# Kernel tuning notes

Measured on AMD Instinct MI355X. Metric: run time of the kernel, lower is better.

The kernel has to match this reference:

```python
import jax, jax.numpy as jnp
import numpy as np

N_HEADS = 16

def setup_inputs() -> dict:
    key = jax.random.key(0)
    ks = jax.random.split(key, 9)
    B, T, C = 2, 2048, 1024
    s = 1.0 / np.sqrt(C)
    return {
        "x": jax.random.normal(ks[0], (B, T, C), dtype=jnp.float32),
        "Wq": jax.random.normal(ks[1], (C, C), dtype=jnp.float32) * s,
        "bq": jax.random.normal(ks[2], (C,), dtype=jnp.float32) * s,
        "Wk": jax.random.normal(ks[3], (C, C), dtype=jnp.float32) * s,
        "bk": jax.random.normal(ks[4], (C,), dtype=jnp.float32) * s,
        "Wv": jax.random.normal(ks[5], (C, C), dtype=jnp.float32) * s,
        "bv": jax.random.normal(ks[6], (C,), dtype=jnp.float32) * s,
        "Wo": jax.random.normal(ks[7], (C, C), dtype=jnp.float32) * s,
        "bo": jax.random.normal(ks[8], (C,), dtype=jnp.float32) * s,
    }

def reference(x, Wq, bq, Wk, bk, Wv, bv, Wo, bo):
    B, T, C = x.shape
    H = N_HEADS
    d = C // H
    # projections -> [B, H, T, d]
    def proj(W, b):
        return (x @ W + b).reshape(B, T, H, d).transpose(0, 2, 1, 3)
    Q, K, V = proj(Wq, bq), proj(Wk, bk), proj(Wv, bv)
    scores = jnp.einsum('bhqd,bhkd->bhqk', Q, K) / jnp.sqrt(jnp.float32(d))
    causal = jnp.tril(jnp.ones((T, T), dtype=bool))  # keep lower triangle
    scores = jnp.where(causal, scores, jnp.finfo(scores.dtype).min)
    attn = jax.nn.softmax(scores, axis=-1)
    out = jnp.einsum('bhqk,bhkd->bhqd', attn, V)  # [B,H,T,d]
    out = out.transpose(0, 2, 1, 3).reshape(B, T, C)
    return out @ Wo + bo
```

## Files before the change

kernel.cpp:

```cpp
#include <hip/hip_runtime.h>
#include <stdint.h>

#define BB 2
#define TT 2048
#define CC 1024
#define HH 16
#define DD 64
#define MM (BB*TT)

typedef unsigned short u16;
typedef __attribute__((ext_vector_type(8))) short short8;
typedef __attribute__((ext_vector_type(4))) float float4v;
typedef __attribute__((ext_vector_type(16))) float f32x16;
typedef __attribute__((ext_vector_type(4))) unsigned short ushort4v;

typedef const __attribute__((address_space(1))) void* gas_t;
typedef __attribute__((address_space(3))) void* las_t;

__device__ __forceinline__ u16 f2bf(float f) {
  union { float f; uint32_t u; } v; v.f = f;
  uint32_t u = v.u;
  return (u16)((u + 0x7FFFu + ((u >> 16) & 1)) >> 16);
}

__device__ __forceinline__ uint32_t cvtpk(float lo, float hi) {
  uint32_t r;
  asm("v_cvt_pk_bf16_f32 %0, %1, %2" : "=v"(r) : "v"(lo), "v"(hi));
  return r;
}

__device__ __forceinline__ void gld_lds16(const void* g, void* l) {
  __builtin_amdgcn_global_load_lds((gas_t)g, (las_t)l, 16, 0, 0);
}

__global__ __launch_bounds__(256) void k_convert_x(const float* __restrict__ x, u16* __restrict__ xb) {
  int i = (blockIdx.x * 256 + threadIdx.x) * 4;
  float4v v = *(const float4v*)(x + i);
  ushort4v o;
  o[0] = f2bf(v[0]); o[1] = f2bf(v[1]); o[2] = f2bf(v[2]); o[3] = f2bf(v[3]);
  *(ushort4v*)(xb + i) = o;
}

__global__ __launch_bounds__(256) void k_transpose_w(const float* __restrict__ Wq, const float* __restrict__ Wk,
                                                     const float* __restrict__ Wv, const float* __restrict__ Wo,
                                                     u16* __restrict__ WT) {
  __shared__ u16 tile[64][72];
  int which = blockIdx.y;
  const float* W = (which == 0) ? Wq : (which == 1) ? Wk : (which == 2) ? Wv : Wo;
  u16* out = WT + (size_t)which * CC * CC;
  int tr = (blockIdx.x >> 4) * 64, tc = (blockIdx.x & 15) * 64;
#pragma unroll
  for (int i = 0; i < 16; ++i) {
    int e = i * 256 + threadIdx.x;
    int r = e >> 6, c = e & 63;
    tile[r][c] = f2bf(W[(size_t)(tr + r) * CC + tc + c]);
  }
  __syncthreads();
#pragma unroll
  for (int i = 0; i < 16; ++i) {
    int e = i * 256 + threadIdx.x;
    int cc2 = e >> 6, rr = e & 63;
    out[(size_t)(tc + cc2) * CC + tr + rr] = tile[rr][cc2];
  }
}

__global__ __launch_bounds__(256, 2) void k_qkv_gemm(
    const u16* __restrict__ xb, const u16* __restrict__ WTall,
    const float* __restrict__ bq, const float* __restrict__ bk, const float* __restrict__ bv,
    u16* __restrict__ Qw, u16* __restrict__ Kw, u16* __restrict__ Vtw) {
  __shared__ u16 Al[2][128 * 32];
  __shared__ u16 Bl[2][128 * 32];
  int p = blockIdx.y;
  const u16* WT = WTall + (size_t)p * (CC * CC);
  const float* bias = (p == 0) ? bq : (p == 1) ? bk : bv;
  int m0 = (blockIdx.x >> 3) * 128;
  int n0 = (blockIdx.x & 7) * 128;
  int tid = threadIdx.x;
  int lane = tid & 63, wave = tid >> 6;
  int wr = wave >> 1, wc = wave & 1;

  float4v acc[4][4];
#pragma unroll
  for (int i = 0; i < 4; ++i)
#pragma unroll
    for (int j = 0; j < 4; ++j) acc[i][j] = float4v{0.f, 0.f, 0.f, 0.f};

  auto stage = [&](int buf, int kt) {
    int k0 = kt * 32;
#pragma unroll
    for (int it = 0; it < 2; ++it) {
      int fc = tid + it * 256;
      int r = fc >> 2, c = fc & 3;
      int cg = c ^ ((r >> 1) & 3);
      const u16* gA = xb + (size_t)(m0 + r) * CC + k0 + cg * 8;
      const u16* gB = WT + (size_t)(n0 + r) * CC + k0 + cg * 8;
      char* lA = (char*)&Al[buf][0] + (wave * 64 + it * 256) * 16;
      char* lB = (char*)&Bl[buf][0] + (wave * 64 + it * 256) * 16;
      gld_lds16(gA, lA);
      gld_lds16(gB, lB);
    }
  };

  stage(0, 0);
  __syncthreads();
  int buf = 0;
  for (int kt = 0; kt < 32; ++kt) {
    if (kt + 1 < 32) stage(buf ^ 1, kt + 1);
    short8 af[4], bfr[4];
#pragma unroll
    for (int mf = 0; mf < 4; ++mf) {
      int row = wr * 64 + mf * 16 + (lane & 15);
      int cs = (lane >> 4) ^ ((row >> 1) & 3);
      af[mf] = *(const short8*)((const char*)&Al[buf][0] + row * 64 + cs * 16);
    }
#pragma unroll
    for (int nf = 0; nf < 4; ++nf) {
      int row = wc * 64 + nf * 16 + (lane & 15);
      int cs = (lane >> 4) ^ ((row >> 1) & 3);
      bfr[nf] = *(const short8*)((const char*)&Bl[buf][0] + row * 64 + cs * 16);
    }
#pragma unroll
    for (int mf = 0; mf < 4; ++mf)
#pragma unroll
      for (int nf = 0; nf < 4; ++nf)
        acc[mf][nf] = __builtin_amdgcn_mfma_f32_16x16x32_bf16(af[mf], bfr[nf], acc[mf][nf], 0, 0, 0);
    __syncthreads();
    buf ^= 1;
  }

  const float QSCALE = 0.125f * 1.44269504088896340736f;
#pragma unroll
  for (int mf = 0; mf < 4; ++mf) {
#pragma unroll
    for (int nf = 0; nf < 4; ++nf) {
      int n = n0 + wc * 64 + nf * 16 + (lane & 15);
      float bval = bias[n];
      int rowBase = wr * 64 + mf * 16 + (lane >> 4) * 4;
      int m_ = m0 + rowBase;
      int b_ = m_ >> 11, t_ = m_ & 2047;
      int h_ = n >> 6, dd = n & 63;
      if (p == 2) {
        ushort4v pk;
#pragma unroll
        for (int i = 0; i < 4; ++i) pk[i] = f2bf(acc[mf][nf][i] + bval);
        *(ushort4v*)(Vtw + ((size_t)(b_ * HH + h_) * DD + dd) * TT + t_) = pk;
      } else {
        u16* outp = (p == 0) ? Qw : Kw;
        float s = (p == 0) ? QSCALE : 1.0f;
#pragma unroll
        for (int i = 0; i < 4; ++i) {
          outp[((size_t)(b_ * HH + h_) * TT + (t_ + i)) * DD + dd] = f2bf((acc[mf][nf][i] + bval) * s);
        }
      }
    }
  }
}

__global__ __launch_bounds__(128, 2) void k_attn(
    const u16* __restrict__ Qw, const u16* __restrict__ Kw,
    const u16* __restrict__ Vtw, u16* __restrict__ Ow) {
  __shared__ u16 Klds[2][64 * 64];
  __shared__ u16 Vlds[2][64 * 64];
  int bid = blockIdx.x;
  int xcd = bid & 7, rank = bid >> 3;
  int bh = xcd + ((rank & 3) << 3);
  int u = 31 - (rank >> 2);
  int tid = threadIdx.x, lane = tid & 63, wave = tid >> 6;
  int l31 = lane & 31, hi = lane >> 5;
  int b_ = bh >> 4, h_ = bh & 15;
  const u16* Qbase = Qw + (size_t)bh * TT * DD;
  const u16* Kbase = Kw + (size_t)bh * TT * DD;
  const u16* Vbase = Vtw + (size_t)bh * DD * TT;
  int qw = u * 64 + wave * 32;
  int nt = u + 1;

  short8 qf[4];
#pragma unroll
  for (int ks = 0; ks < 4; ++ks)
    qf[ks] = *(const short8*)(Qbase + (size_t)(qw + l31) * DD + ks * 16 + hi * 8);

  int sr = tid >> 3;
  int sc = tid & 7;

  f32x16 acc0, acc1;
#pragma unroll
  for (int r = 0; r < 16; ++r) { acc0[r] = 0.f; acc1[r] = 0.f; }
  float mrun = -1e30f, lrun = 0.f;

  auto stageKV = [&](int t, int buf) {
    int kv0 = t * 64;
#pragma unroll
    for (int rd = 0; rd < 4; ++rd) {
      int r = rd * 16 + sr;
      int cg = sc ^ (r & 7);
      const u16* gK = Kbase + (size_t)(kv0 + r) * DD + cg * 8;
      const u16* gV = Vbase + (size_t)r * TT + kv0 + cg * 8;
      char* lK = (char*)&Klds[buf][0] + (rd * 128 + wave * 64) * 16;
      char* lV = (char*)&Vlds[buf][0] + (rd * 128 + wave * 64) * 16;
      gld_lds16(gK, lK);
      gld_lds16(gV, lV);
    }
  };

  stageKV(0, 0);
  int buf = 0;
  for (int t = 0; t < nt; ++t) {
    __syncthreads();
    if (t + 1 < nt) stageKV(t + 1, buf ^ 1);
    int kv0 = t * 64;
    const char* Kb = (const char*)&Klds[buf][0];
    const char* Vb = (const char*)&Vlds[buf][0];
    int swz = (l31 & 7);

    f32x16 s0, s1;
#pragma unroll
    for (int r = 0; r < 16; ++r) { s0[r] = 0.f; s1[r] = 0.f; }
#pragma unroll
    for (int ks = 0; ks < 4; ++ks) {
      short8 kf = *(const short8*)(Kb + l31 * 128 + ((2 * ks + hi) ^ swz) * 16);
      s0 = __builtin_amdgcn_mfma_f32_32x32x16_bf16(kf, qf[ks], s0, 0, 0, 0);
    }
#pragma unroll
    for (int ks = 0; ks < 4; ++ks) {
      short8 kf = *(const short8*)(Kb + (l31 + 32) * 128 + ((2 * ks + hi) ^ swz) * 16);
      s1 = __builtin_amdgcn_mfma_f32_32x32x16_bf16(kf, qf[ks], s1, 0, 0, 0);
    }

    if (kv0 + 63 > qw) {
      int qg = qw + l31;
#pragma unroll
      for (int r = 0; r < 16; ++r) {
        int kvg = kv0 + 8 * (r >> 2) + 4 * hi + (r & 3);
        if (kvg > qg) s0[r] = -1e30f;
        if (kvg + 32 > qg) s1[r] = -1e30f;
      }
    }

    float pm = -1e30f;
#pragma unroll
    for (int r = 0; r < 16; ++r) pm = fmaxf(pm, s0[r]);
#pragma unroll
    for (int r = 0; r < 16; ++r) pm = fmaxf(pm, s1[r]);
    pm = fmaxf(pm, __shfl_xor(pm, 32));

    if (__any(pm > mrun + 8.f)) {
      float mn = fmaxf(mrun, pm);
      float sc_ = __builtin_exp2f(mrun - mn);
      mrun = mn; lrun *= sc_;
#pragma unroll
      for (int r = 0; r < 16; ++r) { acc0[r] *= sc_; acc1[r] *= sc_; }
    }

    float rs = 0.f;
#pragma unroll
    for (int r = 0; r < 16; ++r) { s0[r] = __builtin_exp2f(s0[r] - mrun); rs += s0[r]; }
#pragma unroll
    for (int r = 0; r < 16; ++r) { s1[r] = __builtin_exp2f(s1[r] - mrun); rs += s1[r]; }
    rs += __shfl_xor(rs, 32);
    lrun += rs;

    uint32_t pk0[4][2], pk1[4][2];
#pragma unroll
    for (int m = 0; m < 4; ++m) {
      pk0[m][0] = cvtpk(s0[4 * m + 0], s0[4 * m + 1]);
      pk0[m][1] = cvtpk(s0[4 * m + 2], s0[4 * m + 3]);
      pk1[m][0] = cvtpk(s1[4 * m + 0], s1[4 * m + 1]);
      pk1[m][1] = cvtpk(s1[4 * m + 2], s1[4 * m + 3]);
    }

#define SLICE(PK, Q1, VS)                                                     \
    {                                                                         \
      uint32_t k0 = hi ? PK[2 * Q1 + 1][0] : PK[2 * Q1][0];                   \
      uint32_t k1 = hi ? PK[2 * Q1 + 1][1] : PK[2 * Q1][1];                   \
      uint32_t t0 = hi ? PK[2 * Q1][0] : PK[2 * Q1 + 1][0];                   \
      uint32_t t1 = hi ? PK[2 * Q1][1] : PK[2 * Q1 + 1][1];                   \
      uint32_t r0 = (uint32_t)__shfl_xor((int)t0, 32);                        \
      uint32_t r1 = (uint32_t)__shfl_xor((int)t1, 32);                        \
      union { uint32_t u[4]; short8 v; } pw;                                  \
      pw.u[0] = hi ? r0 : k0; pw.u[1] = hi ? r1 : k1;                         \
      pw.u[2] = hi ? k0 : r0; pw.u[3] = hi ? k1 : r1;                         \
      short8 vf0 = *(const short8*)(Vb + l31 * 128 + ((2 * VS + hi) ^ swz) * 16);       \
      short8 vf1 = *(const short8*)(Vb + (l31 + 32) * 128 + ((2 * VS + hi) ^ swz) * 16);\
      acc0 = __builtin_amdgcn_mfma_f32_32x32x16_bf16(vf0, pw.v, acc0, 0, 0, 0);         \
      acc1 = __builtin_amdgcn_mfma_f32_32x32x16_bf16(vf1, pw.v, acc1, 0, 0, 0);         \
    }
    SLICE(pk0, 0, 0)
    SLICE(pk0, 1, 1)
    SLICE(pk1, 0, 2)
    SLICE(pk1, 1, 3)
#undef SLICE
    buf ^= 1;
  }

  float inv = 1.f / lrun;
  int t_ = qw + l31;
  u16* orow = Ow + ((size_t)(b_ * TT + t_)) * CC + h_ * DD;
#pragma unroll
  for (int m = 0; m < 4; ++m) {
    ushort4v p0, p1;
#pragma unroll
    for (int j = 0; j < 4; ++j) {
      p0[j] = f2bf(acc0[4 * m + j] * inv);
      p1[j] = f2bf(acc1[4 * m + j] * inv);
    }
    *(ushort4v*)(orow + 8 * m + 4 * hi) = p0;
    *(ushort4v*)(orow + 32 + 8 * m + 4 * hi) = p1;
  }
}

__global__ __launch_bounds__(256, 2) void k_out_gemm(
    const u16* __restrict__ Ob, const u16* __restrict__ WoT,
    const float* __restrict__ bo, float* __restrict__ out) {
  __shared__ u16 Al[2][128 * 32];
  __shared__ u16 Bl[2][128 * 32];
  int m0 = (blockIdx.x >> 3) * 128;
  int n0 = (blockIdx.x & 7) * 128;
  int tid = threadIdx.x;
  int lane = tid & 63, wave = tid >> 6;
  int wr = wave >> 1, wc = wave & 1;

  float4v acc[4][4];
#pragma unroll
  for (int i = 0; i < 4; ++i)
#pragma unroll
    for (int j = 0; j < 4; ++j) acc[i][j] = float4v{0.f, 0.f, 0.f, 0.f};

  auto stage = [&](int buf, int kt) {
    int k0 = kt * 32;
#pragma unroll
    for (int it = 0; it < 2; ++it) {
      int fc = tid + it * 256;
      int r = fc >> 2, c = fc & 3;
      int cg = c ^ ((r >> 1) & 3);
      const u16* gA = Ob + (size_t)(m0 + r) * CC + k0 + cg * 8;
      const u16* gB = WoT + (size_t)(n0 + r) * CC + k0 + cg * 8;
      char* lA = (char*)&Al[buf][0] + (wave * 64 + it * 256) * 16;
      char* lB = (char*)&Bl[buf][0] + (wave * 64 + it * 256) * 16;
      gld_lds16(gA, lA);
      gld_lds16(gB, lB);
    }
  };

  stage(0, 0);
  __syncthreads();
  int buf = 0;
  for (int kt = 0; kt < 32; ++kt) {
    if (kt + 1 < 32) stage(buf ^ 1, kt + 1);
    short8 af[4], bfr[4];
#pragma unroll
    for (int mf = 0; mf < 4; ++mf) {
      int row = wr * 64 + mf * 16 + (lane & 15);
      int cs = (lane >> 4) ^ ((row >> 1) & 3);
      af[mf] = *(const short8*)((const char*)&Al[buf][0] + row * 64 + cs * 16);
    }
#pragma unroll
    for (int nf = 0; nf < 4; ++nf) {
      int row = wc * 64 + nf * 16 + (lane & 15);
      int cs = (lane >> 4) ^ ((row >> 1) & 3);
      bfr[nf] = *(const short8*)((const char*)&Bl[buf][0] + row * 64 + cs * 16);
    }
#pragma unroll
    for (int mf = 0; mf < 4; ++mf)
#pragma unroll
      for (int nf = 0; nf < 4; ++nf)
        acc[mf][nf] = __builtin_amdgcn_mfma_f32_16x16x32_bf16(af[mf], bfr[nf], acc[mf][nf], 0, 0, 0);
    __syncthreads();
    buf ^= 1;
  }

#pragma unroll
  for (int mf = 0; mf < 4; ++mf)
#pragma unroll
    for (int nf = 0; nf < 4; ++nf) {
      int n = n0 + wc * 64 + nf * 16 + (lane & 15);
      float bval = bo[n];
      int rowBase = m0 + wr * 64 + mf * 16 + (lane >> 4) * 4;
#pragma unroll
      for (int i = 0; i < 4; ++i)
        out[(size_t)(rowBase + i) * CC + n] = acc[mf][nf][i] + bval;
    }
}

extern "C" void kernel_launch(void* const* d_in, const int* in_sizes, int n_in,
                              void* d_out, int out_size, void* d_ws, size_t ws_size,
                              hipStream_t stream) {
  const float* x  = (const float*)d_in[0];
  const float* Wq = (const float*)d_in[1];
  const float* bq = (const float*)d_in[2];
  const float* Wk = (const float*)d_in[3];
  const float* bk = (const float*)d_in[4];
  const float* Wv = (const float*)d_in[5];
  const float* bv = (const float*)d_in[6];
  const float* Wo = (const float*)d_in[7];
  const float* bo = (const float*)d_in[8];
  float* out = (float*)d_out;
  char* ws = (char*)d_ws;
  if (ws_size < (size_t)50331648) return;

  u16* xb  = (u16*)(ws);
  u16* WT  = (u16*)(ws + 8388608);
  u16* Qw  = (u16*)(ws + 16777216);
  u16* Kw  = (u16*)(ws + 25165824);
  u16* Vtw = (u16*)(ws + 33554432);
  u16* Ob  = (u16*)(ws + 41943040);

  hipLaunchKernelGGL(k_convert_x, dim3(4096), dim3(256), 0, stream, x, xb);
  hipLaunchKernelGGL(k_transpose_w, dim3(256, 4), dim3(256), 0, stream, Wq, Wk, Wv, Wo, WT);
  hipLaunchKernelGGL(k_qkv_gemm, dim3(256, 3), dim3(256), 0, stream,
                     xb, WT, bq, bk, bv, Qw, Kw, Vtw);
  hipLaunchKernelGGL(k_attn, dim3(1024), dim3(128), 0, stream, Qw, Kw, Vtw, Ob);
  hipLaunchKernelGGL(k_out_gemm, dim3(256), dim3(256), 0, stream,
                     Ob, WT + 3 * 1048576, bo, out);
}
```

Before: 204.6 us.

## Split attention KV range across two wave pairs and merge partial softmax states

After: 215.0 us. 1.05x slower.

```diff
diff --git a/kernel.cpp b/kernel.cpp
--- a/kernel.cpp
+++ b/kernel.cpp
@@ -119,32 +119,51 @@
       int cs = (lane >> 4) ^ ((row >> 1) & 3);
       bfr[nf] = *(const short8*)((const char*)&Bl[buf][0] + row * 64 + cs * 16);
     }
-#pragma unroll
-    for (int mf = 0; mf < 4; ++mf)
-#pragma unroll
-      for (int nf = 0; nf < 4; ++nf)
-        acc[mf][nf] = __builtin_amdgcn_mfma_f32_16x16x32_bf16(af[mf], bfr[nf], acc[mf][nf], 0, 0, 0);
+    if (p == 2) {
+#pragma unroll
+      for (int mf = 0; mf < 4; ++mf)
+#pragma unroll
+        for (int nf = 0; nf < 4; ++nf)
+          acc[mf][nf] = __builtin_amdgcn_mfma_f32_16x16x32_bf16(bfr[nf], af[mf], acc[mf][nf], 0, 0, 0);
+    } else {
+#pragma unroll
+      for (int mf = 0; mf < 4; ++mf)
+#pragma unroll
+        for (int nf = 0; nf < 4; ++nf)
+          acc[mf][nf] = __builtin_amdgcn_mfma_f32_16x16x32_bf16(af[mf], bfr[nf], acc[mf][nf], 0, 0, 0);
+    }
     __syncthreads();
     buf ^= 1;
   }
 
   const float QSCALE = 0.125f * 1.44269504088896340736f;
-#pragma unroll
-  for (int mf = 0; mf < 4; ++mf) {
-#pragma unroll
-    for (int nf = 0; nf < 4; ++nf) {
-      int n = n0 + wc * 64 + nf * 16 + (lane & 15);
-      float bval = bias[n];
-      int rowBase = wr * 64 + mf * 16 + (lane >> 4) * 4;
-      int m_ = m0 + rowBase;
-      int b_ = m_ >> 11, t_ = m_ & 2047;
-      int h_ = n >> 6, dd = n & 63;
-      if (p == 2) {
-        ushort4v pk;
-#pragma unroll
-        for (int i = 0; i < 4; ++i) pk[i] = f2bf(acc[mf][nf][i] + bval);
-        *(ushort4v*)(Vtw + ((size_t)(b_ * HH + h_) * DD + dd) * TT + t_) = pk;
-      } else {
+  if (p == 2) {
+#pragma unroll
+    for (int mf = 0; mf < 4; ++mf) {
+#pragma unroll
+      for (int nf = 0; nf < 4; ++nf) {
+        int m_ = m0 + wr * 64 + mf * 16 + (lane & 15);
+        int b_ = m_ >> 11, t_ = m_ & 2047;
+#pragma unroll
+        for (int i = 0; i < 4; ++i) {
+          int nn = n0 + wc * 64 + nf * 16 + (lane >> 4) * 4 + i;
+          float bval = bias[nn];
+          int h_ = nn >> 6, dd = nn & 63;
+          Vtw[((size_t)(b_ * HH + h_) * DD + dd) * TT + t_] = f2bf(acc[mf][nf][i] + bval);
+        }
+      }
+    }
+  } else {
+#pragma unroll
+    for (int mf = 0; mf < 4; ++mf) {
+#pragma unroll
+      for (int nf = 0; nf < 4; ++nf) {
+        int n = n0 + wc * 64 + nf * 16 + (lane & 15);
+        float bval = bias[n];
+        int rowBase = wr * 64 + mf * 16 + (lane >> 4) * 4;
+        int m_ = m0 + rowBase;
+        int b_ = m_ >> 11, t_ = m_ & 2047;
+        int h_ = n >> 6, dd = n & 63;
         u16* outp = (p == 0) ? Qw : Kw;
         float s = (p == 0) ? QSCALE : 1.0f;
 #pragma unroll
@@ -156,38 +175,43 @@
   }
 }
 
-__global__ __launch_bounds__(128, 2) void k_attn(
+__global__ __launch_bounds__(256, 2) void k_attn(
     const u16* __restrict__ Qw, const u16* __restrict__ Kw,
     const u16* __restrict__ Vtw, u16* __restrict__ Ow) {
-  __shared__ u16 Klds[2][64 * 64];
-  __shared__ u16 Vlds[2][64 * 64];
+  __shared__ u16 Klds[2][2][64 * 64];
+  __shared__ u16 Vlds[2][2][64 * 64];
   int bid = blockIdx.x;
   int xcd = bid & 7, rank = bid >> 3;
   int bh = xcd + ((rank & 3) << 3);
   int u = 31 - (rank >> 2);
   int tid = threadIdx.x, lane = tid & 63, wave = tid >> 6;
+  int wq = wave & 1, wk = wave >> 1;
   int l31 = lane & 31, hi = lane >> 5;
   int b_ = bh >> 4, h_ = bh & 15;
   const u16* Qbase = Qw + (size_t)bh * TT * DD;
   const u16* Kbase = Kw + (size_t)bh * TT * DD;
   const u16* Vbase = Vtw + (size_t)bh * DD * TT;
-  int qw = u * 64 + wave * 32;
+  int q32 = u * 64 + wq * 32;
   int nt = u + 1;
+  int hA = (nt + 1) >> 1;
+  int hB = nt >> 1;
+  int tbase = wk ? hA : 0;
+  int myn = wk ? hB : hA;
+  int ptid = wq * 64 + lane;
+  int sr = ptid >> 3, sc = ptid & 7;
+  int swz = l31 & 7;
 
   short8 qf[4];
 #pragma unroll
   for (int ks = 0; ks < 4; ++ks)
-    qf[ks] = *(const short8*)(Qbase + (size_t)(qw + l31) * DD + ks * 16 + hi * 8);
-
-  int sr = tid >> 3;
-  int sc = tid & 7;
+    qf[ks] = *(const short8*)(Qbase + (size_t)(q32 + l31) * DD + ks * 16 + hi * 8);
 
   f32x16 acc0, acc1;
 #pragma unroll
   for (int r = 0; r < 16; ++r) { acc0[r] = 0.f; acc1[r] = 0.f; }
   float mrun = -1e30f, lrun = 0.f;
 
-  auto stageKV = [&](int t, int buf) {
+  auto stageKV = [&](int t, int sb) {
     int kv0 = t * 64;
 #pragma unroll
     for (int rd = 0; rd < 4; ++rd) {
@@ -195,116 +219,140 @@
       int cg = sc ^ (r & 7);
       const u16* gK = Kbase + (size_t)(kv0 + r) * DD + cg * 8;
       const u16* gV = Vbase + (size_t)r * TT + kv0 + cg * 8;
-      char* lK = (char*)&Klds[buf][0] + (rd * 128 + wave * 64) * 16;
-      char* lV = (char*)&Vlds[buf][0] + (rd * 128 + wave * 64) * 16;
+      char* lK = (char*)&Klds[wk][sb][0] + (rd * 128 + wq * 64) * 16;
+      char* lV = (char*)&Vlds[wk][sb][0] + (rd * 128 + wq * 64) * 16;
       gld_lds16(gK, lK);
       gld_lds16(gV, lV);
     }
   };
 
-  stageKV(0, 0);
+  if (myn > 0) stageKV(tbase, 0);
   int buf = 0;
-  for (int t = 0; t < nt; ++t) {
+  for (int i = 0; i < hA; ++i) {
     __syncthreads();
-    if (t + 1 < nt) stageKV(t + 1, buf ^ 1);
-    int kv0 = t * 64;
-    const char* Kb = (const char*)&Klds[buf][0];
-    const char* Vb = (const char*)&Vlds[buf][0];
-    int swz = (l31 & 7);
-
-    f32x16 s0, s1;
-#pragma unroll
-    for (int r = 0; r < 16; ++r) { s0[r] = 0.f; s1[r] = 0.f; }
-#pragma unroll
-    for (int ks = 0; ks < 4; ++ks) {
-      short8 kf = *(const short8*)(Kb + l31 * 128 + ((2 * ks + hi) ^ swz) * 16);
-      s0 = __builtin_amdgcn_mfma_f32_32x32x16_bf16(kf, qf[ks], s0, 0, 0, 0);
-    }
-#pragma unroll
-    for (int ks = 0; ks < 4; ++ks) {
-      short8 kf = *(const short8*)(Kb + (l31 + 32) * 128 + ((2 * ks + hi) ^ swz) * 16);
-      s1 = __builtin_amdgcn_mfma_f32_32x32x16_bf16(kf, qf[ks], s1, 0, 0, 0);
-    }
-
-    if (kv0 + 63 > qw) {
-      int qg = qw + l31;
-#pragma unroll
-      for (int r = 0; r < 16; ++r) {
-        int kvg = kv0 + 8 * (r >> 2) + 4 * hi + (r & 3);
-        if (kvg > qg) s0[r] = -1e30f;
-        if (kvg + 32 > qg) s1[r] = -1e30f;
-      }
-    }
-
-    float pm = -1e30f;
-#pragma unroll
-    for (int r = 0; r < 16; ++r) pm = fmaxf(pm, s0[r]);
-#pragma unroll
-    for (int r = 0; r < 16; ++r) pm = fmaxf(pm, s1[r]);
-    pm = fmaxf(pm, __shfl_xor(pm, 32));
-
-    if (__any(pm > mrun + 8.f)) {
-      float mn = fmaxf(mrun, pm);
-      float sc_ = __builtin_exp2f(mrun - mn);
-      mrun = mn; lrun *= sc_;
-#pragma unroll
-      for (int r = 0; r < 16; ++r) { acc0[r] *= sc_; acc1[r] *= sc_; }
-    }
-
-    float rs = 0.f;
-#pragma unroll
-    for (int r = 0; r < 16; ++r) { s0[r] = __builtin_exp2f(s0[r] - mrun); rs += s0[r]; }
-#pragma unroll
-    for (int r = 0; r < 16; ++r) { s1[r] = __builtin_exp2f(s1[r] - mrun); rs += s1[r]; }
-    rs += __shfl_xor(rs, 32);
-    lrun += rs;
-
-    uint32_t pk0[4][2], pk1[4][2];
+    if (i + 1 < myn) stageKV(tbase + i + 1, buf ^ 1);
+    if (i < myn) {
+      int t = tbase + i;
+      int kv0 = t * 64;
+      const char* Kb = (const char*)&Klds[wk][buf][0];
+      const char* Vb = (const char*)&Vlds[wk][buf][0];
+
+      f32x16 s0, s1;
+#pragma unroll
+      for (int r = 0; r < 16; ++r) { s0[r] = 0.f; s1[r] = 0.f; }
+#pragma unroll
+      for (int ks = 0; ks < 4; ++ks) {
+        short8 kf = *(const short8*)(Kb + l31 * 128 + ((2 * ks + hi) ^ swz) * 16);
+        s0 = __builtin_amdgcn_mfma_f32_32x32x16_bf16(kf, qf[ks], s0, 0, 0, 0);
+      }
+#pragma unroll
+      for (int ks = 0; ks < 4; ++ks) {
+        short8 kf = *(const short8*)(Kb + (l31 + 32) * 128 + ((2 * ks + hi) ^ swz) * 16);
+        s1 = __builtin_amdgcn_mfma_f32_32x32x16_bf16(kf, qf[ks], s1, 0, 0, 0);
+      }
+
+      if (kv0 + 63 > q32) {
+        int qg = q32 + l31;
+#pragma unroll
+        for (int r = 0; r < 16; ++r) {
+          int kvg = kv0 + 8 * (r >> 2) + 4 * hi + (r & 3);
+          if (kvg > qg) s0[r] = -1e30f;
+          if (kvg + 32 > qg) s1[r] = -1e30f;
+        }
+      }
+
+      float pm = -1e30f;
+#pragma unroll
+      for (int r = 0; r < 16; ++r) pm = fmaxf(pm, s0[r]);
+#pragma unroll
+      for (int r = 0; r < 16; ++r) pm = fmaxf(pm, s1[r]);
+      pm = fmaxf(pm, __shfl_xor(pm, 32));
+
+      if (__any(pm > mrun + 8.f)) {
+        float mn = fmaxf(mrun, pm);
+        float sc_ = __builtin_exp2f(mrun - mn);
+        mrun = mn; lrun *= sc_;
+#pragma unroll
+        for (int r = 0; r < 16; ++r) { acc0[r] *= sc_; acc1[r] *= sc_; }
+      }
+
+      float rs = 0.f;
+#pragma unroll
+      for (int r = 0; r < 16; ++r) { s0[r] = __builtin_exp2f(s0[r] - mrun); rs += s0[r]; }
+#pragma unroll
+      for (int r = 0; r < 16; ++r) { s1[r] = __builtin_exp2f(s1[r] - mrun); rs += s1[r]; }
+      rs += __shfl_xor(rs, 32);
+      lrun += rs;
+
+      uint32_t pk0[4][2], pk1[4][2];
+#pragma unroll
+      for (int m = 0; m < 4; ++m) {
+        pk0[m][0] = cvtpk(s0[4 * m + 0], s0[4 * m + 1]);
+        pk0[m][1] = cvtpk(s0[4 * m + 2], s0[4 * m + 3]);
+        pk1[m][0] = cvtpk(s1[4 * m + 0], s1[4 * m + 1]);
+        pk1[m][1] = cvtpk(s1[4 * m + 2], s1[4 * m + 3]);
+      }
+
+#define SLICE(PK, Q1, VS)                                                     \
+      {                                                                       \
+        uint32_t k0 = hi ? PK[2 * Q1 + 1][0] : PK[2 * Q1][0];                 \
+        uint32_t k1 = hi ? PK[2 * Q1 + 1][1] : PK[2 * Q1][1];                 \
+        uint32_t t0 = hi ? PK[2 * Q1][0] : PK[2 * Q1 + 1][0];                 \
+        uint32_t t1 = hi ? PK[2 * Q1][1] : PK[2 * Q1 + 1][1];                 \
+        uint32_t r0 = (uint32_t)__shfl_xor((int)t0, 32);                      \
+        uint32_t r1 = (uint32_t)__shfl_xor((int)t1, 32);                      \
+        union { uint32_t u[4]; short8 v; } pw;                                \
+        pw.u[0] = hi ? r0 : k0; pw.u[1] = hi ? r1 : k1;                       \
+        pw.u[2] = hi ? k0 : r0; pw.u[3] = hi ? k1 : r1;                       \
+        short8 vf0 = *(const short8*)(Vb + l31 * 128 + ((2 * VS + hi) ^ swz) * 16);       \
+        short8 vf1 = *(const short8*)(Vb + (l31 + 32) * 128 + ((2 * VS + hi) ^ swz) * 16);\
+        acc0 = __builtin_amdgcn_mfma_f32_32x32x16_bf16(vf0, pw.v, acc0, 0, 0, 0);         \
+        acc1 = __builtin_amdgcn_mfma_f32_32x32x16_bf16(vf1, pw.v, acc1, 0, 0, 0);         \
+      }
+      SLICE(pk0, 0, 0)
+      SLICE(pk0, 1, 1)
+      SLICE(pk1, 0, 2)
+      SLICE(pk1, 1, 3)
+#undef SLICE
+    }
+    buf ^= 1;
+  }
+
+  __syncthreads();
+  float* Mbuf = (float*)&Klds[0][0][0];
+  if (wk == 1) {
+    float* mp = Mbuf + (size_t)(wq * 64 + lane) * 37;
+    mp[0] = mrun; mp[1] = lrun;
+#pragma unroll
+    for (int r = 0; r < 16; ++r) { mp[2 + r] = acc0[r]; mp[18 + r] = acc1[r]; }
+  }
+  __syncthreads();
+  if (wk == 0) {
+    const float* mp = Mbuf + (size_t)(wq * 64 + lane) * 37;
+    float m1 = mp[0], l1 = mp[1];
+    float mn = fmaxf(mrun, m1);
+    float sA = __builtin_exp2f(mrun - mn);
+    float sB = __builtin_exp2f(m1 - mn);
+    float inv = 1.f / (lrun * sA + l1 * sB);
+    u16* Olds = (u16*)&Vlds[0][0][0] + wq * (32 * 72);
 #pragma unroll
     for (int m = 0; m < 4; ++m) {
-      pk0[m][0] = cvtpk(s0[4 * m + 0], s0[4 * m + 1]);
-      pk0[m][1] = cvtpk(s0[4 * m + 2], s0[4 * m + 3]);
-      pk1[m][0] = cvtpk(s1[4 * m + 0], s1[4 * m + 1]);
-      pk1[m][1] = cvtpk(s1[4 * m + 2], s1[4 * m + 3]);
-    }
-
-#define SLICE(PK, Q1, VS)                                                     \
-    {                                                                         \
-      uint32_t k0 = hi ? PK[2 * Q1 + 1][0] : PK[2 * Q1][0];                   \
-      uint32_t k1 = hi ? PK[2 * Q1 + 1][1] : PK[2 * Q1][1];                   \
-      uint32_t t0 = hi ? PK[2 * Q1][0] : PK[2 * Q1 + 1][0];                   \
-      uint32_t t1 = hi ? PK[2 * Q1][1] : PK[2 * Q1 + 1][1];                   \
-      uint32_t r0 = (uint32_t)__shfl_xor((int)t0, 32);                        \
-      uint32_t r1 = (uint32_t)__shfl_xor((int)t1, 32);                        \
-      union { uint32_t u[4]; short8 v; } pw;                                  \
-      pw.u[0] = hi ? r0 : k0; pw.u[1] = hi ? r1 : k1;                         \
-      pw.u[2] = hi ? k0 : r0; pw.u[3] = hi ? k1 : r1;                         \
-      short8 vf0 = *(const short8*)(Vb + l31 * 128 + ((2 * VS + hi) ^ swz) * 16);       \
-      short8 vf1 = *(const short8*)(Vb + (l31 + 32) * 128 + ((2 * VS + hi) ^ swz) * 16);\
-      acc0 = __builtin_amdgcn_mfma_f32_32x32x16_bf16(vf0, pw.v, acc0, 0, 0, 0);         \
-      acc1 = __builtin_amdgcn_mfma_f32_32x32x16_bf16(vf1, pw.v, acc1, 0, 0, 0);         \
-    }
-    SLICE(pk0, 0, 0)
-    SLICE(pk0, 1, 1)
-    SLICE(pk1, 0, 2)
-    SLICE(pk1, 1, 3)
-#undef SLICE
-    buf ^= 1;
-  }
-
-  float inv = 1.f / lrun;
-  int t_ = qw + l31;
-  u16* orow = Ow + ((size_t)(b_ * TT + t_)) * CC + h_ * DD;
-#pragma unroll
-  for (int m = 0; m < 4; ++m) {
-    ushort4v p0, p1;
-#pragma unroll
-    for (int j = 0; j < 4; ++j) {
-      p0[j] = f2bf(acc0[4 * m + j] * inv);
-      p1[j] = f2bf(acc1[4 * m + j] * inv);
-    }
-    *(ushort4v*)(orow + 8 * m + 4 * hi) = p0;
-    *(ushort4v*)(orow + 32 + 8 * m + 4 * hi) = p1;
+      ushort4v o0, o1;
+#pragma unroll
+      for (int jj = 0; jj < 4; ++jj) {
+        o0[jj] = f2bf((acc0[4 * m + jj] * sA + mp[2 + 4 * m + jj] * sB) * inv);
+        o1[jj] = f2bf((acc1[4 * m + jj] * sA + mp[18 + 4 * m + jj] * sB) * inv);
+      }
+      *(ushort4v*)(Olds + l31 * 72 + 8 * m + 4 * hi) = o0;
+      *(ushort4v*)(Olds + l31 * 72 + 32 + 8 * m + 4 * hi) = o1;
+    }
+    asm volatile("s_waitcnt lgkmcnt(0)" ::: "memory");
+#pragma unroll
+    for (int rr = 0; rr < 4; ++rr) {
+      int q = rr * 8 + (lane >> 3);
+      short8 val = *(const short8*)(Olds + q * 72 + (lane & 7) * 8);
+      *(short8*)(Ow + ((size_t)(b_ * TT + q32 + q)) * CC + h_ * DD + (lane & 7) * 8) = val;
+    }
   }
 }
 
@@ -408,7 +456,7 @@
   hipLaunchKernelGGL(k_transpose_w, dim3(256, 4), dim3(256), 0, stream, Wq, Wk, Wv, Wo, WT);
   hipLaunchKernelGGL(k_qkv_gemm, dim3(256, 3), dim3(256), 0, stream,
                      xb, WT, bq, bk, bv, Qw, Kw, Vtw);
-  hipLaunchKernelGGL(k_attn, dim3(1024), dim3(128), 0, stream, Qw, Kw, Vtw, Ob);
+  hipLaunchKernelGGL(k_attn, dim3(1024), dim3(256), 0, stream, Qw, Kw, Vtw, Ob);
   hipLaunchKernelGGL(k_out_gemm, dim3(256), dim3(256), 0, stream,
                      Ob, WT + 3 * 1048576, bo, out);
 }
```
